# Optimization experiments

Measured on AMD Instinct MI355X. Metric: run time of the kernel, lower is better.

The kernel has to match this reference:

```python
import jax, jax.numpy as jnp
import numpy as np

WINDOW_SIZE = 11
SIGMA = 1.5
C_IN = 3

def _gaussian_window():
    coords = jnp.arange(WINDOW_SIZE, dtype=jnp.float32) - WINDOW_SIZE // 2
    g = jnp.exp(-(coords ** 2) / (2.0 * SIGMA ** 2))
    g = g / g.sum()
    win = g[:, None] * g[None, :]                       # [11, 11]
    return jnp.broadcast_to(win[None, None], (C_IN, 1, WINDOW_SIZE, WINDOW_SIZE))

def _depthwise_conv(x, w):
    pad = WINDOW_SIZE // 2
    return jax.lax.conv_general_dilated(
        x, w,
        window_strides=(1, 1),
        padding=[(pad, pad), (pad, pad)],
        dimension_numbers=('NCHW', 'OIHW', 'NCHW'),
        feature_group_count=C_IN)

def setup_inputs() -> dict:
    key = jax.random.key(0)
    k1, k2 = jax.random.split(key)
    clean = jax.random.uniform(k1, (32, 3, 512, 512), dtype=jnp.float32)
    adversarial = jax.random.uniform(k2, (32, 3, 512, 512), dtype=jnp.float32)
    return {"clean": clean, "adversarial": adversarial}

def reference(clean, adversarial):
    C1 = 0.01 ** 2
    C2 = 0.03 ** 2
    w = _gaussian_window()
    mu1 = _depthwise_conv(clean, w)
    mu2 = _depthwise_conv(adversarial, w)
    mu1_sq = mu1 ** 2
    mu2_sq = mu2 ** 2
    mu12 = mu1 * mu2
    sigma1_sq = _depthwise_conv(clean ** 2, w) - mu1_sq
    sigma2_sq = _depthwise_conv(adversarial ** 2, w) - mu2_sq
    sigma12 = _depthwise_conv(clean * adversarial, w) - mu12
    ssim_map = ((2.0 * mu12 + C1) * (2.0 * sigma12 + C2)) / (
        (mu1_sq + mu2_sq + C1) * (sigma1_sq + sigma2_sq + C2))
    return 1.0 - ssim_map.mean()
```

## Files before the change

### kernel.cpp

```cpp
#include <hip/hip_runtime.h>


typedef float v2f __attribute__((ext_vector_type(2)));
typedef float v4f __attribute__((ext_vector_type(4)));

#define IMG 512
#define TW 64
#define TH 32
#define HALO 5
#define HCOLS 74
#define HSTRIDE 75
#define RPT1 4
#define SEGS 8
#define NPIX 25165824.0

__device__ constexpr float WT[11] = {
    0.00102838f, 0.00759876f, 0.03600077f, 0.10936068f, 0.21300552f,
    0.26601173f,
    0.21300552f, 0.10936068f, 0.03600077f, 0.00759876f, 0.00102838f};

__global__ __launch_bounds__(512)
__attribute__((amdgpu_waves_per_eu(4, 8)))
void ssim_main(const float* __restrict__ clean,
               const float* __restrict__ adv,
               double* __restrict__ accum)
{
    __shared__ __align__(16) v4f hbuf[TH * HSTRIDE];
    __shared__ float wpart[8];

    const int tid = threadIdx.x;
    const int b = blockIdx.x;
    const int plane = b >> 7;
    const int t7 = b & 127;
    const int tile_x = (t7 & 7) * TW;
    const int tile_y = (t7 >> 3) * TH;

    const float* __restrict__ cp = clean + (size_t)plane * (IMG * IMG);
    const float* __restrict__ ap = adv   + (size_t)plane * (IMG * IMG);

    for (int u = tid; u < HCOLS * SEGS; u += 512) {
        const int seg = u / HCOLS;
        const int uc  = u - seg * HCOLS;
        const int col = tile_x + uc - HALO;
        const bool cvalid = ((unsigned)col < IMG);
        const int or0 = seg * RPT1;

        v2f accA[RPT1], accB[RPT1];
        #pragma unroll
        for (int o = 0; o < RPT1; ++o) {
            accA[o] = (v2f){0.f, 0.f};
            accB[o] = (v2f){0.f, 0.f};
        }

        #pragma unroll
        for (int j = 0; j < RPT1 + 10; ++j) {
            const int gr = tile_y + or0 - HALO + j;
            v2f t = {0.f, 0.f};
            if (cvalid && (unsigned)gr < IMG) {
                const int gi = gr * IMG + col;
                const float x = cp[gi];
                const float y = ap[gi];
                t.x = x + y;
                t.y = x - y;
            }
            const v2f p = t * t;
            #pragma unroll
            for (int o = 0; o < RPT1; ++o) {
                const int kv = j - o;
                if (kv >= 0 && kv < 11) {
                    const float w = WT[kv];
                    accA[o] += w * t;
                    accB[o] += w * p;
                }
            }
        }

        #pragma unroll
        for (int o = 0; o < RPT1; ++o) {
            hbuf[(or0 + o) * HSTRIDE + uc] =
                (v4f){accA[o].x, accA[o].y, accB[o].x, accB[o].y};
        }
    }
    __syncthreads();

    const int row = tid & 31;
    const int cs  = tid >> 5;
    const int c0  = cs * 4;
    const v4f* __restrict__ hrow = hbuf + row * HSTRIDE + c0;

    v2f A[4], B[4];
    #pragma unroll
    for (int o = 0; o < 4; ++o) {
        A[o] = (v2f){0.f, 0.f};
        B[o] = (v2f){0.f, 0.f};
    }

    #pragma unroll
    for (int k = 0; k < 14; ++k) {
        const v4f h = hrow[k];
        const v2f hA = {h.x, h.y};
        const v2f hB = {h.z, h.w};
        #pragma unroll
        for (int o = 0; o < 4; ++o) {
            const int kh = k - o;
            if (kh >= 0 && kh < 11) {
                const float w = WT[kh];
                A[o] += w * hA;
                B[o] += w * hB;
            }
        }
    }

    const float C1 = 1e-4f;
    const float C2 = 9e-4f;
    float lsum = 0.f;
    #pragma unroll
    for (int o = 0; o < 4; ++o) {
        const float U = A[o].x * A[o].x;
        const float V = A[o].y * A[o].y;
        const float halfUmV = 0.5f * (U - V);
        const float halfUpV = 0.5f * (U + V);
        const float num1 = halfUmV + C1;
        const float num2 = 0.5f * (B[o].x - B[o].y) - halfUmV + C2;
        const float den1 = halfUpV + C1;
        const float den2 = 0.5f * (B[o].x + B[o].y) - halfUpV + C2;
        lsum += (num1 * num2) * __builtin_amdgcn_rcpf(den1 * den2);
    }

    #pragma unroll
    for (int off = 32; off > 0; off >>= 1)
        lsum += __shfl_down(lsum, off);
    const int lane = tid & 63;
    const int wave = tid >> 6;
    if (lane == 0) wpart[wave] = lsum;
    __syncthreads();
    if (tid == 0) {
        float bs = 0.f;
        #pragma unroll
        for (int w = 0; w < 8; ++w) bs += wpart[w];
        atomicAdd(accum, (double)bs);
    }
}

__global__ void ssim_finalize(const double* __restrict__ accum,
                              float* __restrict__ out)
{
    if (threadIdx.x == 0) {
        out[0] = 1.f - (float)(accum[0] / NPIX);
    }
}

extern "C" void kernel_launch(void* const* d_in, const int* in_sizes, int n_in,
                              void* d_out, int out_size, void* d_ws, size_t ws_size,
                              hipStream_t stream)
{
    const float* clean = (const float*)d_in[0];
    const float* adv   = (const float*)d_in[1];
    float* out = (float*)d_out;
    double* accum = (double*)d_ws;

    hipMemsetAsync(accum, 0, sizeof(double), stream);

    const int nblocks = 96 * 128;
    ssim_main<<<nblocks, 512, 0, stream>>>(clean, adv, accum);
    ssim_finalize<<<1, 64, 0, stream>>>(accum, out);
}
```

Baseline: 364.1 us.

## Halve tile height and batch interior row loads in vertical pass

Measured after the change: 453.6 us. 24.6% more time.

```diff
diff --git a/kernel.cpp b/kernel.cpp
--- a/kernel.cpp
+++ b/kernel.cpp
@@ -6,12 +6,13 @@
 
 #define IMG 512
 #define TW 64
-#define TH 32
+#define TH 16
 #define HALO 5
 #define HCOLS 74
 #define HSTRIDE 75
 #define RPT1 4
-#define SEGS 8
+#define SEGS 4
+#define NROWS 14
 #define NPIX 25165824.0
 
 __device__ constexpr float WT[11] = {
@@ -19,31 +20,60 @@
     0.26601173f,
     0.21300552f, 0.10936068f, 0.03600077f, 0.00759876f, 0.00102838f};
 
-__global__ __launch_bounds__(512)
+__global__ __launch_bounds__(256)
 __attribute__((amdgpu_waves_per_eu(4, 8)))
 void ssim_main(const float* __restrict__ clean,
                const float* __restrict__ adv,
                double* __restrict__ accum)
 {
     __shared__ __align__(16) v4f hbuf[TH * HSTRIDE];
-    __shared__ float wpart[8];
+    __shared__ float wpart[4];
 
     const int tid = threadIdx.x;
     const int b = blockIdx.x;
-    const int plane = b >> 7;
-    const int t7 = b & 127;
-    const int tile_x = (t7 & 7) * TW;
-    const int tile_y = (t7 >> 3) * TH;
+    const int plane = b >> 8;
+    const int t8 = b & 255;
+    const int tile_x = (t8 & 7) * TW;
+    const int tile_y = (t8 >> 3) * TH;
 
     const float* __restrict__ cp = clean + (size_t)plane * (IMG * IMG);
     const float* __restrict__ ap = adv   + (size_t)plane * (IMG * IMG);
 
-    for (int u = tid; u < HCOLS * SEGS; u += 512) {
+    for (int u = tid; u < HCOLS * SEGS; u += 256) {
         const int seg = u / HCOLS;
         const int uc  = u - seg * HCOLS;
         const int col = tile_x + uc - HALO;
         const bool cvalid = ((unsigned)col < IMG);
         const int or0 = seg * RPT1;
+        const int gr0 = tile_y + or0 - HALO;
+
+        v2f t[NROWS];
+        if (cvalid && gr0 >= 0 && gr0 + (NROWS - 1) < IMG) {
+            const float* __restrict__ cpp = cp + (size_t)gr0 * IMG + col;
+            const float* __restrict__ app = ap + (size_t)gr0 * IMG + col;
+            float xs[NROWS], ys[NROWS];
+            #pragma unroll
+            for (int j = 0; j < NROWS; ++j) {
+                xs[j] = cpp[j * IMG];
+                ys[j] = app[j * IMG];
+            }
+            #pragma unroll
+            for (int j = 0; j < NROWS; ++j)
+                t[j] = (v2f){xs[j] + ys[j], xs[j] - ys[j]};
+        } else {
+            #pragma unroll
+            for (int j = 0; j < NROWS; ++j) {
+                const int gr = gr0 + j;
+                v2f v = {0.f, 0.f};
+                if (cvalid && (unsigned)gr < IMG) {
+                    const int gi = gr * IMG + col;
+                    const float x = cp[gi];
+                    const float y = ap[gi];
+                    v = (v2f){x + y, x - y};
+                }
+                t[j] = v;
+            }
+        }
 
         v2f accA[RPT1], accB[RPT1];
         #pragma unroll
@@ -51,25 +81,16 @@
             accA[o] = (v2f){0.f, 0.f};
             accB[o] = (v2f){0.f, 0.f};
         }
-
         #pragma unroll
-        for (int j = 0; j < RPT1 + 10; ++j) {
-            const int gr = tile_y + or0 - HALO + j;
-            v2f t = {0.f, 0.f};
-            if (cvalid && (unsigned)gr < IMG) {
-                const int gi = gr * IMG + col;
-                const float x = cp[gi];
-                const float y = ap[gi];
-                t.x = x + y;
-                t.y = x - y;
-            }
-            const v2f p = t * t;
+        for (int j = 0; j < NROWS; ++j) {
+            const v2f tv = t[j];
+            const v2f p = tv * tv;
             #pragma unroll
             for (int o = 0; o < RPT1; ++o) {
                 const int kv = j - o;
                 if (kv >= 0 && kv < 11) {
                     const float w = WT[kv];
-                    accA[o] += w * t;
+                    accA[o] += w * tv;
                     accB[o] += w * p;
                 }
             }
@@ -83,8 +104,8 @@
     }
     __syncthreads();
 
-    const int row = tid & 31;
-    const int cs  = tid >> 5;
+    const int row = tid & 15;
+    const int cs  = tid >> 4;
     const int c0  = cs * 4;
     const v4f* __restrict__ hrow = hbuf + row * HSTRIDE + c0;
 
@@ -137,7 +158,7 @@
     if (tid == 0) {
         float bs = 0.f;
         #pragma unroll
-        for (int w = 0; w < 8; ++w) bs += wpart[w];
+        for (int w = 0; w < 4; ++w) bs += wpart[w];
         atomicAdd(accum, (double)bs);
     }
 }
@@ -161,7 +182,7 @@
 
     hipMemsetAsync(accum, 0, sizeof(double), stream);
 
-    const int nblocks = 96 * 128;
-    ssim_main<<<nblocks, 512, 0, stream>>>(clean, adv, accum);
+    const int nblocks = 96 * 256;
+    ssim_main<<<nblocks, 256, 0, stream>>>(clean, adv, accum);
     ssim_finalize<<<1, 64, 0, stream>>>(accum, out);
 }
```

## Stage input tile in LDS and halve tile height for more blocks

Applied to the files above, without the earlier changes.

Result: slower. 453.1 us (+24.4%).

```diff
diff --git a/kernel.cpp b/kernel.cpp
--- a/kernel.cpp
+++ b/kernel.cpp
@@ -6,12 +6,14 @@
 
 #define IMG 512
 #define TW 64
-#define TH 32
+#define TH 16
 #define HALO 5
-#define HCOLS 74
+#define SROWS 26
+#define SCOLS 74
+#define SSTRIDE 76
 #define HSTRIDE 75
-#define RPT1 4
-#define SEGS 8
+#define RPTV 2
+#define VSEGS 8
 #define NPIX 25165824.0
 
 __device__ constexpr float WT[11] = {
@@ -20,52 +22,57 @@
     0.21300552f, 0.10936068f, 0.03600077f, 0.00759876f, 0.00102838f};
 
 __global__ __launch_bounds__(512)
-__attribute__((amdgpu_waves_per_eu(4, 8)))
 void ssim_main(const float* __restrict__ clean,
                const float* __restrict__ adv,
                double* __restrict__ accum)
 {
+    __shared__ __align__(16) v2f stg[SROWS * SSTRIDE];
     __shared__ __align__(16) v4f hbuf[TH * HSTRIDE];
     __shared__ float wpart[8];
 
     const int tid = threadIdx.x;
     const int b = blockIdx.x;
-    const int plane = b >> 7;
-    const int t7 = b & 127;
-    const int tile_x = (t7 & 7) * TW;
-    const int tile_y = (t7 >> 3) * TH;
+    const int plane = b >> 8;
+    const int t8 = b & 255;
+    const int tile_x = (t8 & 7) * TW;
+    const int tile_y = (t8 >> 3) * TH;
 
     const float* __restrict__ cp = clean + (size_t)plane * (IMG * IMG);
     const float* __restrict__ ap = adv   + (size_t)plane * (IMG * IMG);
 
-    for (int u = tid; u < HCOLS * SEGS; u += 512) {
-        const int seg = u / HCOLS;
-        const int uc  = u - seg * HCOLS;
-        const int col = tile_x + uc - HALO;
-        const bool cvalid = ((unsigned)col < IMG);
-        const int or0 = seg * RPT1;
+    for (int idx = tid; idx < SROWS * SCOLS; idx += 512) {
+        const int r = idx / SCOLS;
+        const int c = idx - r * SCOLS;
+        const int gr = tile_y + r - HALO;
+        const int gc = tile_x + c - HALO;
+        v2f v = {0.f, 0.f};
+        if ((unsigned)gr < IMG && (unsigned)gc < IMG) {
+            const int gi = gr * IMG + gc;
+            const float x = cp[gi];
+            const float y = ap[gi];
+            v = (v2f){x + y, x - y};
+        }
+        stg[r * SSTRIDE + c] = v;
+    }
+    __syncthreads();
 
-        v2f accA[RPT1], accB[RPT1];
+    for (int u = tid; u < SCOLS * VSEGS; u += 512) {
+        const int seg = u / SCOLS;
+        const int uc  = u - seg * SCOLS;
+        const int or0 = seg * RPTV;
+
+        v2f accA[RPTV], accB[RPTV];
         #pragma unroll
-        for (int o = 0; o < RPT1; ++o) {
+        for (int o = 0; o < RPTV; ++o) {
             accA[o] = (v2f){0.f, 0.f};
             accB[o] = (v2f){0.f, 0.f};
         }
-
         #pragma unroll
-        for (int j = 0; j < RPT1 + 10; ++j) {
-            const int gr = tile_y + or0 - HALO + j;
-            v2f t = {0.f, 0.f};
-            if (cvalid && (unsigned)gr < IMG) {
-                const int gi = gr * IMG + col;
-                const float x = cp[gi];
-                const float y = ap[gi];
-                t.x = x + y;
-                t.y = x - y;
-            }
+        for (int j = 0; j < RPTV + 10; ++j) {
+            const v2f t = stg[(or0 + j) * SSTRIDE + uc];
             const v2f p = t * t;
             #pragma unroll
-            for (int o = 0; o < RPT1; ++o) {
+            for (int o = 0; o < RPTV; ++o) {
                 const int kv = j - o;
                 if (kv >= 0 && kv < 11) {
                     const float w = WT[kv];
@@ -74,34 +81,32 @@
                 }
             }
         }
-
         #pragma unroll
-        for (int o = 0; o < RPT1; ++o) {
+        for (int o = 0; o < RPTV; ++o) {
             hbuf[(or0 + o) * HSTRIDE + uc] =
                 (v4f){accA[o].x, accA[o].y, accB[o].x, accB[o].y};
         }
     }
     __syncthreads();
 
-    const int row = tid & 31;
-    const int cs  = tid >> 5;
-    const int c0  = cs * 4;
+    const int row = tid & 15;
+    const int cs  = tid >> 4;
+    const int c0  = cs * 2;
     const v4f* __restrict__ hrow = hbuf + row * HSTRIDE + c0;
 
-    v2f A[4], B[4];
+    v2f A[2], B[2];
     #pragma unroll
-    for (int o = 0; o < 4; ++o) {
+    for (int o = 0; o < 2; ++o) {
         A[o] = (v2f){0.f, 0.f};
         B[o] = (v2f){0.f, 0.f};
     }
-
     #pragma unroll
-    for (int k = 0; k < 14; ++k) {
+    for (int k = 0; k < 12; ++k) {
         const v4f h = hrow[k];
         const v2f hA = {h.x, h.y};
         const v2f hB = {h.z, h.w};
         #pragma unroll
-        for (int o = 0; o < 4; ++o) {
+        for (int o = 0; o < 2; ++o) {
             const int kh = k - o;
             if (kh >= 0 && kh < 11) {
                 const float w = WT[kh];
@@ -115,7 +120,7 @@
     const float C2 = 9e-4f;
     float lsum = 0.f;
     #pragma unroll
-    for (int o = 0; o < 4; ++o) {
+    for (int o = 0; o < 2; ++o) {
         const float U = A[o].x * A[o].x;
         const float V = A[o].y * A[o].y;
         const float halfUmV = 0.5f * (U - V);
@@ -161,7 +166,7 @@
 
     hipMemsetAsync(accum, 0, sizeof(double), stream);
 
-    const int nblocks = 96 * 128;
+    const int nblocks = 96 * 256;
     ssim_main<<<nblocks, 512, 0, stream>>>(clean, adv, accum);
     ssim_finalize<<<1, 64, 0, stream>>>(accum, out);
 }
```
